# Kernel tuning notes

Measured on AMD Instinct MI355X. Metric: run time of the kernel, lower is better.

## Reference

```python
import jax, jax.numpy as jnp
import numpy as np

B, T, NH, HD = 2, 2048, 12, 128
HIDDEN = NH * HD
EPS = 1.1920928955078125e-07  # torch fp32 finfo eps (F.rms_norm default)


def _rope_cos_sin(T, d_half, base=10000.0):
    inv = 1.0 / (base ** (jnp.arange(d_half, dtype=jnp.float32) / d_half))
    t = jnp.arange(T, dtype=jnp.float32)
    f = t[:, None] * inv[None, :]  # [T, d_half]
    return jnp.cos(f)[None, :, None, :], jnp.sin(f)[None, :, None, :]


def apply_rotary_emb(x, cos, sin):
    d = x.shape[3] // 2
    x1, x2 = x[..., :d], x[..., d:]
    return jnp.concatenate([x1 * cos + x2 * sin, x1 * -sin + x2 * cos], axis=3)


def rms_norm(x):
    return x * jax.lax.rsqrt(jnp.mean(x * x, axis=-1, keepdims=True) + EPS)


def setup_inputs() -> dict:
    key = jax.random.key(0)
    ks = jax.random.split(key, 5)
    x = jax.random.normal(ks[0], (B, T, HIDDEN), dtype=jnp.float32)
    cos, sin = _rope_cos_sin(T, HD // 2)
    s = 1.0 / np.sqrt(HIDDEN)
    Wq = jax.random.normal(ks[1], (HIDDEN, HIDDEN), dtype=jnp.float32) * s
    Wk = jax.random.normal(ks[2], (HIDDEN, HIDDEN), dtype=jnp.float32) * s
    Wv = jax.random.normal(ks[3], (HIDDEN, HIDDEN), dtype=jnp.float32) * s
    Wp = jax.random.normal(ks[4], (HIDDEN, HIDDEN), dtype=jnp.float32) * s
    return {"x": x, "cos": cos, "sin": sin, "Wq": Wq, "Wk": Wk, "Wv": Wv,
            "Wp": Wp, "window": 1024}


def reference(x, cos, sin, Wq, Wk, Wv, Wp, window):
    Bx, Tx, _ = x.shape
    q = (x @ Wq.T).reshape(Bx, Tx, NH, HD)
    k = (x @ Wk.T).reshape(Bx, Tx, NH, HD)
    v = (x @ Wv.T).reshape(Bx, Tx, NH, HD)
    q = rms_norm(apply_rotary_emb(q, cos, sin))
    k = rms_norm(apply_rotary_emb(k, cos, sin))
    # causal + sliding-window attention (dense, matching the sdpa fallback)
    scale = 1.0 / np.sqrt(HD)
    scores = jnp.einsum('bqhd,bkhd->bhqk', q, k) * scale
    row = jnp.arange(Tx)[:, None]
    col = jnp.arange(Tx)[None, :]
    mask = (col <= row) & (row - col <= window)
    scores = jnp.where(mask[None, None], scores, jnp.finfo(scores.dtype).min)
    attn = jax.nn.softmax(scores, axis=-1)
    y = jnp.einsum('bhqk,bkhd->bqhd', attn, v).reshape(Bx, Tx, HIDDEN)
    return y @ Wp.T
```

## Files before the change

### kernel.cpp

```cpp
#include <hip/hip_runtime.h>
#include <stdint.h>

#define HIDDEN 1536
#define NHEAD 12
#define HD 128
#define TSEQ 2048
#define NROWS 4096
#define KDIM HIDDEN
#define EPS_F 1.1920928955078125e-07f
#define SCALE_LOG2E 0.12751879110195655f
#define FIXSUB 16.6f

typedef unsigned short u16;
typedef __bf16 bf16x8_t __attribute__((ext_vector_type(8)));
typedef float f32x4_t __attribute__((ext_vector_type(4)));

#define MFMA16(a, b, c) __builtin_amdgcn_mfma_f32_16x16x32_bf16((a), (b), (c), 0, 0, 0)
#define GLL(srcp, dstp) \
  __builtin_amdgcn_global_load_lds((const __attribute__((address_space(1))) void*)(srcp), \
                                   (__attribute__((address_space(3))) void*)(dstp), 16, 0, 0)

__device__ __forceinline__ u16 f2bf(float f) {
  unsigned u = __builtin_bit_cast(unsigned, f);
  u = (u + 0x7fffu + ((u >> 16) & 1u)) >> 16;
  return (u16)u;
}
__device__ __forceinline__ float bfu(u16 v) {
  return __builtin_bit_cast(float, ((unsigned)v) << 16);
}

__global__ __launch_bounds__(256) void cast_kernel(const float* __restrict__ in,
                                                   u16* __restrict__ out, int n) {
  int i = (blockIdx.x * 256 + threadIdx.x) * 4;
  if (i >= n) return;
  float4 v = *reinterpret_cast<const float4*>(in + i);
  uint2 pk;
  pk.x = (unsigned)f2bf(v.x) | ((unsigned)f2bf(v.y) << 16);
  pk.y = (unsigned)f2bf(v.z) | ((unsigned)f2bf(v.w) << 16);
  *reinterpret_cast<uint2*>(out + i) = pk;
}

__global__ __launch_bounds__(256) void cast4_kernel(
    const float* __restrict__ a, const float* __restrict__ b, const float* __restrict__ c,
    const float* __restrict__ d, u16* __restrict__ oa, u16* __restrict__ ob,
    u16* __restrict__ oc, u16* __restrict__ od, int n) {
  const float* in;
  u16* out;
  switch (blockIdx.y) {
    case 0: in = a; out = oa; break;
    case 1: in = b; out = ob; break;
    case 2: in = c; out = oc; break;
    default: in = d; out = od; break;
  }
  int i = (blockIdx.x * 256 + threadIdx.x) * 4;
  if (i >= n) return;
  float4 v = *reinterpret_cast<const float4*>(in + i);
  uint2 pk;
  pk.x = (unsigned)f2bf(v.x) | ((unsigned)f2bf(v.y) << 16);
  pk.y = (unsigned)f2bf(v.z) | ((unsigned)f2bf(v.w) << 16);
  *reinterpret_cast<uint2*>(out + i) = pk;
}

__device__ __forceinline__ void gemm_mainloop64(const u16* __restrict__ A,
                                                const u16* __restrict__ W, int M0, int N0,
                                                u16* lds, f32x4_t acc[4][4], int tid) {
  const int w = tid >> 6, l = tid & 63;
  const int lrow = l & 15, kg = l >> 4;
  const int wr = (w >> 1) * 64, wc = (w & 1) * 64;
  const int row0 = tid >> 3, j0 = tid & 7;
  const unsigned jsw = (unsigned)((j0 ^ (row0 & 7)) * 8);
  unsigned offA = (unsigned)((M0 + row0) * KDIM) + jsw;
  unsigned offW = (unsigned)((N0 + row0) * KDIM) + jsw;
  const u16* A1 = A + 32 * KDIM; const u16* A2 = A + 64 * KDIM; const u16* A3 = A + 96 * KDIM;
  const u16* W1 = W + 32 * KDIM; const u16* W2 = W + 64 * KDIM; const u16* W3 = W + 96 * KDIM;
  auto issue = [&](int buf) {
    u16* da = lds + buf * 8192 + w * 512;
    u16* dw = lds + 16384 + buf * 8192 + w * 512;
    GLL(A + offA, da);          GLL(A1 + offA, da + 2048);
    GLL(A2 + offA, da + 4096);  GLL(A3 + offA, da + 6144);
    GLL(W + offW, dw);          GLL(W1 + offW, dw + 2048);
    GLL(W2 + offW, dw + 4096);  GLL(W3 + offW, dw + 6144);
    offA += 64; offW += 64;
  };
  issue(0);
  const int NT = KDIM / 64;
#pragma unroll 1
  for (int kt = 0; kt < NT; ++kt) {
    const int cur = kt & 1;
    if (kt + 1 < NT) {
      issue(cur ^ 1);
      asm volatile("s_waitcnt vmcnt(8)" ::: "memory");
    } else {
      asm volatile("s_waitcnt vmcnt(0)" ::: "memory");
    }
    __builtin_amdgcn_s_barrier();
    asm volatile("" ::: "memory");
    const u16* Ab = lds + cur * 8192;
    const u16* Wb = lds + 16384 + cur * 8192;
#pragma unroll
    for (int s = 0; s < 2; ++s) {
      bf16x8_t af[4], bf_[4];
#pragma unroll
      for (int mi = 0; mi < 4; ++mi) {
        const int row = wr + mi * 16 + lrow;
        af[mi] = *reinterpret_cast<const bf16x8_t*>(Ab + row * 64 +
                                                    (((s << 2) | kg) ^ (row & 7)) * 8);
      }
#pragma unroll
      for (int ni = 0; ni < 4; ++ni) {
        const int row = wc + ni * 16 + lrow;
        bf_[ni] = *reinterpret_cast<const bf16x8_t*>(Wb + row * 64 +
                                                     (((s << 2) | kg) ^ (row & 7)) * 8);
      }
#pragma unroll
      for (int mi = 0; mi < 4; ++mi)
#pragma unroll
        for (int ni = 0; ni < 4; ++ni)
          acc[mi][ni] = MFMA16(af[mi], bf_[ni], acc[mi][ni]);
    }
    asm volatile("s_waitcnt lgkmcnt(0)" ::: "memory");
    __builtin_amdgcn_s_barrier();
    asm volatile("" ::: "memory");
  }
}

__global__ __launch_bounds__(256) void gemm_qkv_kernel(
    const u16* __restrict__ xb, const u16* __restrict__ wq, const u16* __restrict__ wk,
    const u16* __restrict__ wv, const float* __restrict__ cosp, const float* __restrict__ sinp,
    u16* __restrict__ qh, u16* __restrict__ kh, u16* __restrict__ vt) {
  __shared__ __align__(16) u16 lds[32768];
  const int tid = threadIdx.x;
  const int wgid = blockIdx.x;
  const int xcd = wgid & 7, c = wgid >> 3;
  const int m = ((xcd & 3) << 3) + (c & 7);
  const int nz = ((xcd >> 2) * 18) + (c >> 3);
  const int z = nz / 12, n = nz % 12;
  const int M0 = m * 128, N0 = n * 128;
  const u16* W = (z == 0) ? wq : (z == 1) ? wk : wv;
  f32x4_t acc[4][4] = {};
  gemm_mainloop64(xb, W, M0, N0, lds, acc, tid);
  const int w = tid >> 6, l = tid & 63;
  const int lrow = l & 15, kg = l >> 4;
  const int wr = (w >> 1) * 64, wc = (w & 1) * 64;
  char* cs = reinterpret_cast<char*>(lds);
  if (z == 2) {
#pragma unroll
    for (int mi = 0; mi < 4; ++mi)
#pragma unroll
      for (int ni = 0; ni < 4; ++ni)
#pragma unroll
        for (int r = 0; r < 4; ++r) {
          const int t_l = wr + mi * 16 + kg * 4 + r;
          const int d = wc + ni * 16 + lrow;
          const int bofs = (d * 256 + t_l * 2) ^ ((d & 7) << 4);
          *reinterpret_cast<u16*>(cs + bofs) = f2bf(acc[mi][ni][r]);
        }
  } else {
#pragma unroll
    for (int mi = 0; mi < 4; ++mi)
#pragma unroll
      for (int ni = 0; ni < 4; ++ni)
#pragma unroll
        for (int r = 0; r < 4; ++r) {
          const int t_l = wr + mi * 16 + kg * 4 + r;
          const int d = wc + ni * 16 + lrow;
          const int bofs = (t_l * 256 + d * 2) ^ ((t_l & 7) << 4);
          *reinterpret_cast<u16*>(cs + bofs) = f2bf(acc[mi][ni][r]);
        }
  }
  __syncthreads();
  const int rr = tid >> 1, hh = tid & 1;
  const int bb = M0 >> 11;
  const int t0 = M0 & (TSEQ - 1);
  const size_t bhn = (size_t)(bb * NHEAD + n);
  if (z == 2) {
    u16* dst = vt + (bhn * HD + rr) * TSEQ + t0 + hh * 64;
    const char* base = cs + rr * 256 + hh * 128;
#pragma unroll
    for (int j = 0; j < 8; ++j) {
      uint4 v = *reinterpret_cast<const uint4*>(base + ((j ^ (rr & 7)) * 16));
      *reinterpret_cast<uint4*>(dst + j * 8) = v;
    }
  } else {
    const int t = t0 + rr;
    const float* cosb = cosp + t * 64;
    const float* sinb = sinp + t * 64;
    const char* base = cs + rr * 256;
    float ss = 0.0f;
    unsigned pk[32];
#pragma unroll
    for (int j = 0; j < 8; ++j) {
      const int jp = (j ^ (rr & 7)) * 16;
      uint4 vo = *reinterpret_cast<const uint4*>(base + hh * 128 + jp);
      uint4 vx = *reinterpret_cast<const uint4*>(base + (hh ^ 1) * 128 + jp);
      const unsigned vo32[4] = {vo.x, vo.y, vo.z, vo.w};
      const unsigned vx32[4] = {vx.x, vx.y, vx.z, vx.w};
      const float* cj = cosb + j * 8;
      const float* sj = sinb + j * 8;
#pragma unroll
      for (int q2 = 0; q2 < 4; ++q2) {
        float o0 = bfu((u16)(vo32[q2] & 0xffffu)), o1 = bfu((u16)(vo32[q2] >> 16));
        float x0 = bfu((u16)(vx32[q2] & 0xffffu)), x1 = bfu((u16)(vx32[q2] >> 16));
        float cc0 = cj[q2 * 2], cc1 = cj[q2 * 2 + 1];
        float s0 = sj[q2 * 2], s1 = sj[q2 * 2 + 1];
        float y0 = hh ? __builtin_fmaf(o0, cc0, -x0 * s0) : __builtin_fmaf(o0, cc0, x0 * s0);
        float y1 = hh ? __builtin_fmaf(o1, cc1, -x1 * s1) : __builtin_fmaf(o1, cc1, x1 * s1);
        ss = __builtin_fmaf(y0, y0, __builtin_fmaf(y1, y1, ss));
        pk[j * 4 + q2] = (unsigned)f2bf(y0) | ((unsigned)f2bf(y1) << 16);
      }
    }
    ss += __shfl_xor(ss, 1, 64);
    const float rinv = rsqrtf(ss * (1.0f / 128.0f) + EPS_F);
    u16* dst = ((z == 0) ? qh : kh) + (bhn * TSEQ + t) * HD + hh * 64;
#pragma unroll
    for (int j = 0; j < 8; ++j) {
      unsigned o[4];
#pragma unroll
      for (int q2 = 0; q2 < 4; ++q2) {
        float y0 = bfu((u16)(pk[j * 4 + q2] & 0xffffu)) * rinv;
        float y1 = bfu((u16)(pk[j * 4 + q2] >> 16)) * rinv;
        o[q2] = (unsigned)f2bf(y0) | ((unsigned)f2bf(y1) << 16);
      }
      uint4 v;
      v.x = o[0]; v.y = o[1]; v.z = o[2]; v.w = o[3];
      *reinterpret_cast<uint4*>(dst + j * 8) = v;
    }
  }
}

__global__ __launch_bounds__(256) void gemm_out_kernel(const u16* __restrict__ yh,
                                                       const u16* __restrict__ wp,
                                                       float* __restrict__ out) {
  __shared__ __align__(16) u16 lds[32768];
  const int tid = threadIdx.x;
  const int wgid = blockIdx.x;
  const int xcd = wgid & 7, c = wgid >> 3;
  const int m = ((xcd & 3) << 3) + (c & 7);
  const int n = ((xcd >> 2) * 6) + (c >> 3);
  const int M0 = m * 128, N0 = n * 128;
  f32x4_t acc[4][4] = {};
  gemm_mainloop64(yh, wp, M0, N0, lds, acc, tid);
  const int w = tid >> 6, l = tid & 63;
  const int lrow = l & 15, kg = l >> 4;
  const int wr = (w >> 1) * 64, wc = (w & 1) * 64;
#pragma unroll
  for (int mi = 0; mi < 4; ++mi)
#pragma unroll
    for (int ni = 0; ni < 4; ++ni)
#pragma unroll
      for (int r = 0; r < 4; ++r) {
        const int grow = M0 + wr + mi * 16 + kg * 4 + r;
        const int gcol = N0 + wc + ni * 16 + lrow;
        out[(size_t)grow * HIDDEN + gcol] = acc[mi][ni][r];
      }
}

__global__ __launch_bounds__(512, 4) void attn_kernel(const u16* __restrict__ qh,
                                                      const u16* __restrict__ kh,
                                                      const u16* __restrict__ vt,
                                                      u16* __restrict__ yh,
                                                      const int* __restrict__ winp) {
  __shared__ __align__(16) u16 Kl[2][8192];
  __shared__ __align__(16) u16 Vl[2][8192];
  __shared__ __align__(16) u16 Pl[8][1024];
  const int tid = threadIdx.x, w = tid >> 6, l = tid & 63;
  const int lrow = l & 15, kg = l >> 4;
  const int bid = blockIdx.x;
  const int swz = (bid & 7) * 48 + (bid >> 3);
  const int qb = swz & 15;
  const int bh = swz >> 4;
  const int h = bh % NHEAD, b = bh / NHEAD;
  const int win = winp[0];
  const u16* Q = qh + (size_t)bh * TSEQ * HD;
  const u16* K = kh + (size_t)bh * TSEQ * HD;
  const u16* V = vt + (size_t)bh * HD * TSEQ;
  const int qw = qb * 128 + w * 16;
  bf16x8_t aq[4];
#pragma unroll
  for (int ks = 0; ks < 4; ++ks)
    aq[ks] = *reinterpret_cast<const bf16x8_t*>(Q + (qw + lrow) * HD + ks * 32 + kg * 8);
  float lsum[4] = {0.f, 0.f, 0.f, 0.f};
  f32x4_t accv[8] = {};
  int lo = qb * 128 - win;
  if (lo < 0) lo = 0;
  lo &= ~63;
  const int last = qb * 128 + 64;

  u16* Pw = &Pl[w][0];

  auto stage_k = [&](int kv, int buf) {
#pragma unroll
    for (int i = 0; i < 2; ++i) {
      const int c = i * 512 + w * 64 + l;
      const int row = c >> 4, j = c & 15;
      const u16* src = K + (size_t)(kv + row) * HD + ((j ^ (row & 7)) * 8);
      GLL(src, &Kl[buf][0] + i * 4096 + w * 512);
    }
  };
  auto stage_v = [&](int kv, int buf) {
#pragma unroll
    for (int i = 0; i < 2; ++i) {
      const int c = i * 512 + w * 64 + l;
      const int row = c >> 3, j = c & 7;
      const u16* src = V + (size_t)row * TSEQ + kv + ((j ^ (row & 7)) * 8);
      GLL(src, &Vl[buf][0] + i * 4096 + w * 512);
    }
  };

  stage_k(lo, 0);
  stage_v(lo, 0);
  int it = 0;
  for (int kv = lo; kv <= last; kv += 64, ++it) {
    const int cur = it & 1;
    const int kpre = (kv + 64 <= last) ? kv + 64 : last;
    stage_k(kpre, cur ^ 1);
    asm volatile("s_waitcnt vmcnt(2)" ::: "memory");
    __builtin_amdgcn_s_barrier();
    asm volatile("" ::: "memory");
    stage_v(kpre, cur ^ 1);
    const u16* Kb = &Kl[cur][0];
    f32x4_t s[4] = {};
#pragma unroll
    for (int n = 0; n < 4; ++n) {
      const int row = n * 16 + lrow;
#pragma unroll
      for (int ks = 0; ks < 4; ++ks) {
        bf16x8_t bk = *reinterpret_cast<const bf16x8_t*>(
            Kb + row * 128 + (((ks << 2) | kg) ^ (row & 7)) * 8);
        s[n] = MFMA16(aq[ks], bk, s[n]);
      }
    }
    float ps[4][4];
    const bool interior = (kv + 63 <= qw) && ((qw + 15) - kv <= win);
    if (interior) {
#pragma unroll
      for (int n = 0; n < 4; ++n)
#pragma unroll
        for (int r = 0; r < 4; ++r)
          ps[n][r] = exp2f(__builtin_fmaf(s[n][r], SCALE_LOG2E, -FIXSUB));
    } else {
#pragma unroll
      for (int n = 0; n < 4; ++n) {
        const int key = kv + n * 16 + lrow;
#pragma unroll
        for (int r = 0; r < 4; ++r) {
          const int rowq = qw + kg * 4 + r;
          const bool ok = (key <= rowq) && (rowq - key <= win);
          ps[n][r] = ok ? exp2f(__builtin_fmaf(s[n][r], SCALE_LOG2E, -FIXSUB)) : 0.0f;
        }
      }
    }
#pragma unroll
    for (int r = 0; r < 4; ++r)
      lsum[r] += (ps[0][r] + ps[1][r]) + (ps[2][r] + ps[3][r]);
#pragma unroll
    for (int n = 0; n < 4; ++n)
#pragma unroll
      for (int r = 0; r < 4; ++r) {
        const int rp = kg * 4 + r;
        int bofs = rp * 128 + (n * 16 + lrow) * 2;
        bofs ^= (rp & 7) << 4;
        *reinterpret_cast<u16*>(reinterpret_cast<char*>(Pw) + bofs) = f2bf(ps[n][r]);
      }
    asm volatile("s_waitcnt lgkmcnt(0)" ::: "memory");
    __builtin_amdgcn_s_barrier();
    asm volatile("" ::: "memory");
    bf16x8_t ap[2];
#pragma unroll
    for (int k2 = 0; k2 < 2; ++k2) {
      int bofs = lrow * 128 + k2 * 64 + kg * 16;
      bofs ^= (lrow & 7) << 4;
      ap[k2] = *reinterpret_cast<const bf16x8_t*>(reinterpret_cast<const char*>(Pw) + bofs);
    }
    const u16* Vb = &Vl[cur][0];
#pragma unroll
    for (int k2 = 0; k2 < 2; ++k2)
#pragma unroll
      for (int dn = 0; dn < 8; ++dn) {
        const int row = dn * 16 + lrow;
        bf16x8_t bv = *reinterpret_cast<const bf16x8_t*>(
            Vb + row * 64 + (((k2 << 2) | kg) ^ (row & 7)) * 8);
        accv[dn] = MFMA16(ap[k2], bv, accv[dn]);
      }
  }
#pragma unroll
  for (int off = 1; off < 16; off <<= 1)
#pragma unroll
    for (int r = 0; r < 4; ++r) lsum[r] += __shfl_xor(lsum[r], off, 64);
  float inv[4];
#pragma unroll
  for (int r = 0; r < 4; ++r) inv[r] = 1.0f / lsum[r];
#pragma unroll
  for (int dn = 0; dn < 8; ++dn)
#pragma unroll
    for (int r = 0; r < 4; ++r) {
      const int rowg = b * TSEQ + qw + kg * 4 + r;
      const int col = h * HD + dn * 16 + lrow;
      yh[(size_t)rowg * HIDDEN + col] = f2bf(accv[dn][r] * inv[r]);
    }
}

extern "C" void kernel_launch(void* const* d_in, const int* in_sizes, int n_in, void* d_out,
                              int out_size, void* d_ws, size_t ws_size, hipStream_t stream) {
  const float* x = (const float*)d_in[0];
  const float* cosp = (const float*)d_in[1];
  const float* sinp = (const float*)d_in[2];
  const float* Wq = (const float*)d_in[3];
  const float* Wk = (const float*)d_in[4];
  const float* Wv = (const float*)d_in[5];
  const float* Wp = (const float*)d_in[6];
  const int* winp = (const int*)d_in[7];

  char* ws = (char*)d_ws;
  size_t off = 0;
  auto alloc = [&](size_t bytes) {
    char* p = ws + off;
    off += (bytes + 255) & ~(size_t)255;
    return p;
  };
  u16* xb = (u16*)alloc((size_t)NROWS * HIDDEN * 2);
  u16* wqb = (u16*)alloc((size_t)HIDDEN * HIDDEN * 2);
  u16* wkb = (u16*)alloc((size_t)HIDDEN * HIDDEN * 2);
  u16* wvb = (u16*)alloc((size_t)HIDDEN * HIDDEN * 2);
  u16* wpb = (u16*)alloc((size_t)HIDDEN * HIDDEN * 2);
  u16* qh = (u16*)alloc((size_t)NROWS * HIDDEN * 2);
  u16* kh = (u16*)alloc((size_t)NROWS * HIDDEN * 2);
  u16* vt = (u16*)alloc((size_t)NROWS * HIDDEN * 2);
  u16* yh = (u16*)alloc((size_t)NROWS * HIDDEN * 2);

  const int nx = NROWS * HIDDEN;
  const int nw = HIDDEN * HIDDEN;
  cast_kernel<<<nx / 1024, 256, 0, stream>>>(x, xb, nx);
  cast4_kernel<<<dim3(nw / 1024, 4), 256, 0, stream>>>(Wq, Wk, Wv, Wp, wqb, wkb, wvb, wpb, nw);

  gemm_qkv_kernel<<<dim3(1152), 256, 0, stream>>>(xb, wqb, wkb, wvb, cosp, sinp, qh, kh, vt);
  attn_kernel<<<dim3(384), 512, 0, stream>>>(qh, kh, vt, yh, winp);
  gemm_out_kernel<<<dim3(384), 256, 0, stream>>>(yh, wpb, (float*)d_out);
}
```

Measured before the change: 185.9 us.

## Rewrite QKV GEMM with 256x128 tiles, 8 waves and split-phase prefetch

The QKV projection GEMM now uses 256x128 output tiles computed by 512-thread blocks (8 waves), halving the grid and reusing each weight tile across twice as many rows. The main loop is split into two MFMA phases, with the global-to-LDS loads for the next tile issued between them and s_setprio raising wave priority during MFMA bursts, so memory traffic overlaps compute. The RoPE/RMSNorm epilogue and the V transpose are adapted to the larger tile. This is meant to cut global/L2 traffic and improve overlap, at the cost of more LDS per block (96 KB) and more barriers per K-step.

```diff
diff --git a/kernel.cpp b/kernel.cpp
--- a/kernel.cpp
+++ b/kernel.cpp
@@ -59,6 +59,192 @@
   pk.x = (unsigned)f2bf(v.x) | ((unsigned)f2bf(v.y) << 16);
   pk.y = (unsigned)f2bf(v.z) | ((unsigned)f2bf(v.w) << 16);
   *reinterpret_cast<uint2*>(out + i) = pk;
+}
+
+__global__ __launch_bounds__(512, 2) void gemm_qkv_kernel(
+    const u16* __restrict__ xb, const u16* __restrict__ wq, const u16* __restrict__ wk,
+    const u16* __restrict__ wv, const float* __restrict__ cosp, const float* __restrict__ sinp,
+    u16* __restrict__ qh, u16* __restrict__ kh, u16* __restrict__ vt) {
+  __shared__ __align__(16) u16 lds[49152];
+  const int tid = threadIdx.x;
+  const int bid = blockIdx.x;
+  const int xcd = bid & 7, cc = bid >> 3;
+  const int m = xcd * 2 + (cc & 1);
+  const int nz = cc >> 1;
+  const int z = nz / 12, n = nz % 12;
+  const int M0 = m * 256, N0 = n * 128;
+  const u16* W = (z == 0) ? wq : (z == 1) ? wk : wv;
+  const int w = tid >> 6, l = tid & 63;
+  const int lrow = l & 15, kg = l >> 4;
+  const int wm = w >> 1, wn = w & 1;
+  const int srow = tid >> 3;
+  const unsigned jsw = (unsigned)(((tid & 7) ^ (srow & 7)) * 8);
+  const u16* pA0 = xb + (size_t)(M0 + srow) * KDIM + jsw;
+  const u16* pA1 = xb + (size_t)(M0 + 128 + srow) * KDIM + jsw;
+  const u16* pB = W + (size_t)(N0 + srow) * KDIM + jsw;
+  const size_t R64 = (size_t)64 * KDIM;
+  u16* dst0 = lds + w * 512;
+  auto stage = [&](const u16* p, int buf, int i) {
+    u16* db = dst0 + buf * 24576 + i * 8192;
+    GLL(p, db);
+    GLL(p + R64, db + 4096);
+  };
+  stage(pA0, 0, 0);
+  stage(pA1, 0, 1);
+  stage(pB, 0, 2);
+  pA0 += 64; pA1 += 64; pB += 64;
+  asm volatile("s_waitcnt vmcnt(0)" ::: "memory");
+  __builtin_amdgcn_s_barrier();
+  asm volatile("" ::: "memory");
+  f32x4_t acc[4][4] = {};
+  const int aoff = (wm >> 1) * 8192;
+  const int arow0 = (wm & 1) * 64;
+  const int swz = lrow & 7;
+  const int NT = KDIM / 64;
+#pragma unroll 1
+  for (int T = 0; T < NT; ++T) {
+    const int buf = T & 1;
+    const u16* Ab = lds + buf * 24576 + aoff;
+    const u16* Bb = lds + buf * 24576 + 16384;
+    bf16x8_t bfr[4][2], afr[2][2];
+#pragma unroll
+    for (int nf = 0; nf < 4; ++nf)
+#pragma unroll
+      for (int ks = 0; ks < 2; ++ks)
+        bfr[nf][ks] = *reinterpret_cast<const bf16x8_t*>(
+            Bb + (wn * 64 + nf * 16 + lrow) * 64 + (((ks << 2) | kg) ^ swz) * 8);
+#pragma unroll
+    for (int mf = 0; mf < 2; ++mf)
+#pragma unroll
+      for (int ks = 0; ks < 2; ++ks)
+        afr[mf][ks] = *reinterpret_cast<const bf16x8_t*>(
+            Ab + (arow0 + mf * 16 + lrow) * 64 + (((ks << 2) | kg) ^ swz) * 8);
+    if (T + 1 < NT) {
+      stage(pA0, buf ^ 1, 0);
+      stage(pA1, buf ^ 1, 1);
+    }
+    __builtin_amdgcn_s_barrier();
+    asm volatile("" ::: "memory");
+    __builtin_amdgcn_s_setprio(1);
+#pragma unroll
+    for (int mf = 0; mf < 2; ++mf)
+#pragma unroll
+      for (int nf = 0; nf < 4; ++nf)
+#pragma unroll
+        for (int ks = 0; ks < 2; ++ks)
+          acc[mf][nf] = MFMA16(afr[mf][ks], bfr[nf][ks], acc[mf][nf]);
+    __builtin_amdgcn_s_setprio(0);
+    __builtin_amdgcn_s_barrier();
+    asm volatile("" ::: "memory");
+    bf16x8_t afr2[2][2];
+#pragma unroll
+    for (int mf = 0; mf < 2; ++mf)
+#pragma unroll
+      for (int ks = 0; ks < 2; ++ks)
+        afr2[mf][ks] = *reinterpret_cast<const bf16x8_t*>(
+            Ab + (arow0 + (mf + 2) * 16 + lrow) * 64 + (((ks << 2) | kg) ^ swz) * 8);
+    if (T + 1 < NT) {
+      stage(pB, buf ^ 1, 2);
+      pA0 += 64; pA1 += 64; pB += 64;
+    }
+    __builtin_amdgcn_s_barrier();
+    asm volatile("" ::: "memory");
+    __builtin_amdgcn_s_setprio(1);
+#pragma unroll
+    for (int mf = 0; mf < 2; ++mf)
+#pragma unroll
+      for (int nf = 0; nf < 4; ++nf)
+#pragma unroll
+        for (int ks = 0; ks < 2; ++ks)
+          acc[mf + 2][nf] = MFMA16(afr2[mf][ks], bfr[nf][ks], acc[mf + 2][nf]);
+    __builtin_amdgcn_s_setprio(0);
+    asm volatile("s_waitcnt vmcnt(0)" ::: "memory");
+    __builtin_amdgcn_s_barrier();
+    asm volatile("" ::: "memory");
+  }
+  char* cs = reinterpret_cast<char*>(lds);
+  const int bb = M0 >> 11;
+  const int t0 = M0 & (TSEQ - 1);
+  const size_t bhn = (size_t)(bb * NHEAD + n);
+  if (z == 2) {
+#pragma unroll
+    for (int mf = 0; mf < 4; ++mf)
+#pragma unroll
+      for (int nf = 0; nf < 4; ++nf)
+#pragma unroll
+        for (int r = 0; r < 4; ++r) {
+          const int trow = wm * 64 + mf * 16 + kg * 4 + r;
+          const int d = wn * 64 + nf * 16 + lrow;
+          const int bofs = (d * 512 + trow * 2) ^ ((d & 7) << 4);
+          *reinterpret_cast<u16*>(cs + bofs) = f2bf(acc[mf][nf][r]);
+        }
+    __syncthreads();
+    const int d = tid >> 2, tq = tid & 3;
+    u16* dst = vt + (bhn * HD + d) * TSEQ + t0 + tq * 64;
+    const char* rb = cs + d * 512 + tq * 128;
+#pragma unroll
+    for (int j = 0; j < 8; ++j) {
+      uint4 v = *reinterpret_cast<const uint4*>(rb + ((j ^ (d & 7)) * 16));
+      *reinterpret_cast<uint4*>(dst + j * 8) = v;
+    }
+  } else {
+#pragma unroll
+    for (int mf = 0; mf < 4; ++mf)
+#pragma unroll
+      for (int nf = 0; nf < 4; ++nf)
+#pragma unroll
+        for (int r = 0; r < 4; ++r) {
+          const int trow = wm * 64 + mf * 16 + kg * 4 + r;
+          const int d = wn * 64 + nf * 16 + lrow;
+          const int bofs = (trow * 256 + d * 2) ^ ((trow & 7) << 4);
+          *reinterpret_cast<u16*>(cs + bofs) = f2bf(acc[mf][nf][r]);
+        }
+    __syncthreads();
+    const int rr = tid >> 1, hh = tid & 1;
+    const int t = t0 + rr;
+    const float* cosb = cosp + t * 64;
+    const float* sinb = sinp + t * 64;
+    const char* base = cs + rr * 256;
+    float ss = 0.0f;
+    unsigned pk[32];
+#pragma unroll
+    for (int j = 0; j < 8; ++j) {
+      const int jp = (j ^ (rr & 7)) * 16;
+      uint4 vo = *reinterpret_cast<const uint4*>(base + hh * 128 + jp);
+      uint4 vx = *reinterpret_cast<const uint4*>(base + (hh ^ 1) * 128 + jp);
+      const unsigned vo32[4] = {vo.x, vo.y, vo.z, vo.w};
+      const unsigned vx32[4] = {vx.x, vx.y, vx.z, vx.w};
+      const float* cj = cosb + j * 8;
+      const float* sj = sinb + j * 8;
+#pragma unroll
+      for (int q2 = 0; q2 < 4; ++q2) {
+        float o0 = bfu((u16)(vo32[q2] & 0xffffu)), o1 = bfu((u16)(vo32[q2] >> 16));
+        float x0 = bfu((u16)(vx32[q2] & 0xffffu)), x1 = bfu((u16)(vx32[q2] >> 16));
+        float cc0 = cj[q2 * 2], cc1 = cj[q2 * 2 + 1];
+        float s0 = sj[q2 * 2], s1 = sj[q2 * 2 + 1];
+        float y0 = hh ? __builtin_fmaf(o0, cc0, -x0 * s0) : __builtin_fmaf(o0, cc0, x0 * s0);
+        float y1 = hh ? __builtin_fmaf(o1, cc1, -x1 * s1) : __builtin_fmaf(o1, cc1, x1 * s1);
+        ss = __builtin_fmaf(y0, y0, __builtin_fmaf(y1, y1, ss));
+        pk[j * 4 + q2] = (unsigned)f2bf(y0) | ((unsigned)f2bf(y1) << 16);
+      }
+    }
+    ss += __shfl_xor(ss, 1, 64);
+    const float rinv = rsqrtf(ss * (1.0f / 128.0f) + EPS_F);
+    u16* dst = ((z == 0) ? qh : kh) + (bhn * TSEQ + t) * HD + hh * 64;
+#pragma unroll
+    for (int j = 0; j < 8; ++j) {
+      unsigned o[4];
+#pragma unroll
+      for (int q2 = 0; q2 < 4; ++q2) {
+        float y0 = bfu((u16)(pk[j * 4 + q2] & 0xffffu)) * rinv;
+        float y1 = bfu((u16)(pk[j * 4 + q2] >> 16)) * rinv;
+        o[q2] = (unsigned)f2bf(y0) | ((unsigned)f2bf(y1) << 16);
+      }
+      uint4 v;
+      v.x = o[0]; v.y = o[1]; v.z = o[2]; v.w = o[3];
+      *reinterpret_cast<uint4*>(dst + j * 8) = v;
+    }
+  }
 }
 
 __device__ __forceinline__ void gemm_mainloop64(const u16* __restrict__ A,
@@ -124,110 +310,6 @@
   }
 }
 
-__global__ __launch_bounds__(256) void gemm_qkv_kernel(
-    const u16* __restrict__ xb, const u16* __restrict__ wq, const u16* __restrict__ wk,
-    const u16* __restrict__ wv, const float* __restrict__ cosp, const float* __restrict__ sinp,
-    u16* __restrict__ qh, u16* __restrict__ kh, u16* __restrict__ vt) {
-  __shared__ __align__(16) u16 lds[32768];
-  const int tid = threadIdx.x;
-  const int wgid = blockIdx.x;
-  const int xcd = wgid & 7, c = wgid >> 3;
-  const int m = ((xcd & 3) << 3) + (c & 7);
-  const int nz = ((xcd >> 2) * 18) + (c >> 3);
-  const int z = nz / 12, n = nz % 12;
-  const int M0 = m * 128, N0 = n * 128;
-  const u16* W = (z == 0) ? wq : (z == 1) ? wk : wv;
-  f32x4_t acc[4][4] = {};
-  gemm_mainloop64(xb, W, M0, N0, lds, acc, tid);
-  const int w = tid >> 6, l = tid & 63;
-  const int lrow = l & 15, kg = l >> 4;
-  const int wr = (w >> 1) * 64, wc = (w & 1) * 64;
-  char* cs = reinterpret_cast<char*>(lds);
-  if (z == 2) {
-#pragma unroll
-    for (int mi = 0; mi < 4; ++mi)
-#pragma unroll
-      for (int ni = 0; ni < 4; ++ni)
-#pragma unroll
-        for (int r = 0; r < 4; ++r) {
-          const int t_l = wr + mi * 16 + kg * 4 + r;
-          const int d = wc + ni * 16 + lrow;
-          const int bofs = (d * 256 + t_l * 2) ^ ((d & 7) << 4);
-          *reinterpret_cast<u16*>(cs + bofs) = f2bf(acc[mi][ni][r]);
-        }
-  } else {
-#pragma unroll
-    for (int mi = 0; mi < 4; ++mi)
-#pragma unroll
-      for (int ni = 0; ni < 4; ++ni)
-#pragma unroll
-        for (int r = 0; r < 4; ++r) {
-          const int t_l = wr + mi * 16 + kg * 4 + r;
-          const int d = wc + ni * 16 + lrow;
-          const int bofs = (t_l * 256 + d * 2) ^ ((t_l & 7) << 4);
-          *reinterpret_cast<u16*>(cs + bofs) = f2bf(acc[mi][ni][r]);
-        }
-  }
-  __syncthreads();
-  const int rr = tid >> 1, hh = tid & 1;
-  const int bb = M0 >> 11;
-  const int t0 = M0 & (TSEQ - 1);
-  const size_t bhn = (size_t)(bb * NHEAD + n);
-  if (z == 2) {
-    u16* dst = vt + (bhn * HD + rr) * TSEQ + t0 + hh * 64;
-    const char* base = cs + rr * 256 + hh * 128;
-#pragma unroll
-    for (int j = 0; j < 8; ++j) {
-      uint4 v = *reinterpret_cast<const uint4*>(base + ((j ^ (rr & 7)) * 16));
-      *reinterpret_cast<uint4*>(dst + j * 8) = v;
-    }
-  } else {
-    const int t = t0 + rr;
-    const float* cosb = cosp + t * 64;
-    const float* sinb = sinp + t * 64;
-    const char* base = cs + rr * 256;
-    float ss = 0.0f;
-    unsigned pk[32];
-#pragma unroll
-    for (int j = 0; j < 8; ++j) {
-      const int jp = (j ^ (rr & 7)) * 16;
-      uint4 vo = *reinterpret_cast<const uint4*>(base + hh * 128 + jp);
-      uint4 vx = *reinterpret_cast<const uint4*>(base + (hh ^ 1) * 128 + jp);
-      const unsigned vo32[4] = {vo.x, vo.y, vo.z, vo.w};
-      const unsigned vx32[4] = {vx.x, vx.y, vx.z, vx.w};
-      const float* cj = cosb + j * 8;
-      const float* sj = sinb + j * 8;
-#pragma unroll
-      for (int q2 = 0; q2 < 4; ++q2) {
-        float o0 = bfu((u16)(vo32[q2] & 0xffffu)), o1 = bfu((u16)(vo32[q2] >> 16));
-        float x0 = bfu((u16)(vx32[q2] & 0xffffu)), x1 = bfu((u16)(vx32[q2] >> 16));
-        float cc0 = cj[q2 * 2], cc1 = cj[q2 * 2 + 1];
-        float s0 = sj[q2 * 2], s1 = sj[q2 * 2 + 1];
-        float y0 = hh ? __builtin_fmaf(o0, cc0, -x0 * s0) : __builtin_fmaf(o0, cc0, x0 * s0);
-        float y1 = hh ? __builtin_fmaf(o1, cc1, -x1 * s1) : __builtin_fmaf(o1, cc1, x1 * s1);
-        ss = __builtin_fmaf(y0, y0, __builtin_fmaf(y1, y1, ss));
-        pk[j * 4 + q2] = (unsigned)f2bf(y0) | ((unsigned)f2bf(y1) << 16);
-      }
-    }
-    ss += __shfl_xor(ss, 1, 64);
-    const float rinv = rsqrtf(ss * (1.0f / 128.0f) + EPS_F);
-    u16* dst = ((z == 0) ? qh : kh) + (bhn * TSEQ + t) * HD + hh * 64;
-#pragma unroll
-    for (int j = 0; j < 8; ++j) {
-      unsigned o[4];
-#pragma unroll
-      for (int q2 = 0; q2 < 4; ++q2) {
-        float y0 = bfu((u16)(pk[j * 4 + q2] & 0xffffu)) * rinv;
-        float y1 = bfu((u16)(pk[j * 4 + q2] >> 16)) * rinv;
-        o[q2] = (unsigned)f2bf(y0) | ((unsigned)f2bf(y1) << 16);
-      }
-      uint4 v;
-      v.x = o[0]; v.y = o[1]; v.z = o[2]; v.w = o[3];
-      *reinterpret_cast<uint4*>(dst + j * 8) = v;
-    }
-  }
-}
-
 __global__ __launch_bounds__(256) void gemm_out_kernel(const u16* __restrict__ yh,
                                                        const u16* __restrict__ wp,
                                                        float* __restrict__ out) {
@@ -433,7 +515,7 @@
   cast_kernel<<<nx / 1024, 256, 0, stream>>>(x, xb, nx);
   cast4_kernel<<<dim3(nw / 1024, 4), 256, 0, stream>>>(Wq, Wk, Wv, Wp, wqb, wkb, wvb, wpb, nw);
 
-  gemm_qkv_kernel<<<dim3(1152), 256, 0, stream>>>(xb, wqb, wkb, wvb, cosp, sinp, qh, kh, vt);
+  gemm_qkv_kernel<<<dim3(576), 512, 0, stream>>>(xb, wqb, wkb, wvb, cosp, sinp, qh, kh, vt);
   attn_kernel<<<dim3(384), 512, 0, stream>>>(qh, kh, vt, yh, winp);
   gemm_out_kernel<<<dim3(384), 256, 0, stream>>>(yh, wpb, (float*)d_out);
 }
```

New measurement: 203.8 us. 1.1x slower.

## Use 8 waves per GEMM block with 64x32 warp tiles

Applied to the files above, without the earlier changes.

Both GEMM kernels move from 4 waves at 64x64 per wave to 8 waves at 64x32 per wave on the same 128x128 tile. Global-to-LDS loads are split over twice as many threads, and the RoPE/RMSNorm and V-transpose epilogues are redistributed across 512 threads with an extra shuffle for the row norm. This halves per-thread accumulators to raise occupancy and latency hiding, at the cost of more LDS fragment reads per MFMA, since A fragments are now reused across only 2 columns.

```diff
diff --git a/kernel.cpp b/kernel.cpp
--- a/kernel.cpp
+++ b/kernel.cpp
@@ -63,24 +63,25 @@
 
 __device__ __forceinline__ void gemm_mainloop64(const u16* __restrict__ A,
                                                 const u16* __restrict__ W, int M0, int N0,
-                                                u16* lds, f32x4_t acc[4][4], int tid) {
+                                                u16* lds, f32x4_t acc[4][2], int tid) {
   const int w = tid >> 6, l = tid & 63;
   const int lrow = l & 15, kg = l >> 4;
-  const int wr = (w >> 1) * 64, wc = (w & 1) * 64;
+  const int wm = w >> 2, wn = w & 3;
+  const int rbase = wm * 64, cbase = wn * 32;
   const int row0 = tid >> 3, j0 = tid & 7;
   const unsigned jsw = (unsigned)((j0 ^ (row0 & 7)) * 8);
   unsigned offA = (unsigned)((M0 + row0) * KDIM) + jsw;
   unsigned offW = (unsigned)((N0 + row0) * KDIM) + jsw;
-  const u16* A1 = A + 32 * KDIM; const u16* A2 = A + 64 * KDIM; const u16* A3 = A + 96 * KDIM;
-  const u16* W1 = W + 32 * KDIM; const u16* W2 = W + 64 * KDIM; const u16* W3 = W + 96 * KDIM;
+  const size_t R64 = (size_t)64 * KDIM;
   auto issue = [&](int buf) {
     u16* da = lds + buf * 8192 + w * 512;
     u16* dw = lds + 16384 + buf * 8192 + w * 512;
-    GLL(A + offA, da);          GLL(A1 + offA, da + 2048);
-    GLL(A2 + offA, da + 4096);  GLL(A3 + offA, da + 6144);
-    GLL(W + offW, dw);          GLL(W1 + offW, dw + 2048);
-    GLL(W2 + offW, dw + 4096);  GLL(W3 + offW, dw + 6144);
-    offA += 64; offW += 64;
+    GLL(A + offA, da);
+    GLL(A + offA + R64, da + 4096);
+    GLL(W + offW, dw);
+    GLL(W + offW + R64, dw + 4096);
+    offA += 64;
+    offW += 64;
   };
   issue(0);
   const int NT = KDIM / 64;
@@ -89,7 +90,7 @@
     const int cur = kt & 1;
     if (kt + 1 < NT) {
       issue(cur ^ 1);
-      asm volatile("s_waitcnt vmcnt(8)" ::: "memory");
+      asm volatile("s_waitcnt vmcnt(4)" ::: "memory");
     } else {
       asm volatile("s_waitcnt vmcnt(0)" ::: "memory");
     }
@@ -99,23 +100,23 @@
     const u16* Wb = lds + 16384 + cur * 8192;
 #pragma unroll
     for (int s = 0; s < 2; ++s) {
-      bf16x8_t af[4], bf_[4];
+      bf16x8_t af[4], bf_[2];
 #pragma unroll
       for (int mi = 0; mi < 4; ++mi) {
-        const int row = wr + mi * 16 + lrow;
+        const int row = rbase + mi * 16 + lrow;
         af[mi] = *reinterpret_cast<const bf16x8_t*>(Ab + row * 64 +
                                                     (((s << 2) | kg) ^ (row & 7)) * 8);
       }
 #pragma unroll
-      for (int ni = 0; ni < 4; ++ni) {
-        const int row = wc + ni * 16 + lrow;
+      for (int ni = 0; ni < 2; ++ni) {
+        const int row = cbase + ni * 16 + lrow;
         bf_[ni] = *reinterpret_cast<const bf16x8_t*>(Wb + row * 64 +
                                                      (((s << 2) | kg) ^ (row & 7)) * 8);
       }
 #pragma unroll
       for (int mi = 0; mi < 4; ++mi)
 #pragma unroll
-        for (int ni = 0; ni < 4; ++ni)
+        for (int ni = 0; ni < 2; ++ni)
           acc[mi][ni] = MFMA16(af[mi], bf_[ni], acc[mi][ni]);
     }
     asm volatile("s_waitcnt lgkmcnt(0)" ::: "memory");
@@ -124,7 +125,7 @@
   }
 }
 
-__global__ __launch_bounds__(256) void gemm_qkv_kernel(
+__global__ __launch_bounds__(512, 4) void gemm_qkv_kernel(
     const u16* __restrict__ xb, const u16* __restrict__ wq, const u16* __restrict__ wk,
     const u16* __restrict__ wv, const float* __restrict__ cosp, const float* __restrict__ sinp,
     u16* __restrict__ qh, u16* __restrict__ kh, u16* __restrict__ vt) {
@@ -137,21 +138,21 @@
   const int z = nz / 12, n = nz % 12;
   const int M0 = m * 128, N0 = n * 128;
   const u16* W = (z == 0) ? wq : (z == 1) ? wk : wv;
-  f32x4_t acc[4][4] = {};
+  f32x4_t acc[4][2] = {};
   gemm_mainloop64(xb, W, M0, N0, lds, acc, tid);
   const int w = tid >> 6, l = tid & 63;
   const int lrow = l & 15, kg = l >> 4;
-  const int wr = (w >> 1) * 64, wc = (w & 1) * 64;
+  const int wm = w >> 2, wn = w & 3;
   char* cs = reinterpret_cast<char*>(lds);
   if (z == 2) {
 #pragma unroll
     for (int mi = 0; mi < 4; ++mi)
 #pragma unroll
-      for (int ni = 0; ni < 4; ++ni)
+      for (int ni = 0; ni < 2; ++ni)
 #pragma unroll
         for (int r = 0; r < 4; ++r) {
-          const int t_l = wr + mi * 16 + kg * 4 + r;
-          const int d = wc + ni * 16 + lrow;
+          const int t_l = wm * 64 + mi * 16 + kg * 4 + r;
+          const int d = wn * 32 + ni * 16 + lrow;
           const int bofs = (d * 256 + t_l * 2) ^ ((d & 7) << 4);
           *reinterpret_cast<u16*>(cs + bofs) = f2bf(acc[mi][ni][r]);
         }
@@ -159,40 +160,44 @@
 #pragma unroll
     for (int mi = 0; mi < 4; ++mi)
 #pragma unroll
-      for (int ni = 0; ni < 4; ++ni)
+      for (int ni = 0; ni < 2; ++ni)
 #pragma unroll
         for (int r = 0; r < 4; ++r) {
-          const int t_l = wr + mi * 16 + kg * 4 + r;
-          const int d = wc + ni * 16 + lrow;
+          const int t_l = wm * 64 + mi * 16 + kg * 4 + r;
+          const int d = wn * 32 + ni * 16 + lrow;
           const int bofs = (t_l * 256 + d * 2) ^ ((t_l & 7) << 4);
           *reinterpret_cast<u16*>(cs + bofs) = f2bf(acc[mi][ni][r]);
         }
   }
   __syncthreads();
-  const int rr = tid >> 1, hh = tid & 1;
   const int bb = M0 >> 11;
   const int t0 = M0 & (TSEQ - 1);
   const size_t bhn = (size_t)(bb * NHEAD + n);
   if (z == 2) {
-    u16* dst = vt + (bhn * HD + rr) * TSEQ + t0 + hh * 64;
-    const char* base = cs + rr * 256 + hh * 128;
-#pragma unroll
-    for (int j = 0; j < 8; ++j) {
-      uint4 v = *reinterpret_cast<const uint4*>(base + ((j ^ (rr & 7)) * 16));
+    const int dd = tid >> 2, tq = tid & 3;
+    u16* dst = vt + (bhn * HD + dd) * TSEQ + t0 + tq * 32;
+    const char* rb = cs + dd * 256;
+#pragma unroll
+    for (int j = 0; j < 4; ++j) {
+      const int jj = tq * 4 + j;
+      uint4 v = *reinterpret_cast<const uint4*>(rb + ((jj ^ (dd & 7)) * 16));
       *reinterpret_cast<uint4*>(dst + j * 8) = v;
     }
   } else {
+    const int rr = tid >> 2, qd = tid & 3;
+    const int hh = qd >> 1;
     const int t = t0 + rr;
-    const float* cosb = cosp + t * 64;
-    const float* sinb = sinp + t * 64;
+    const float* cosb = cosp + t * 64 + (qd & 1) * 32;
+    const float* sinb = sinp + t * 64 + (qd & 1) * 32;
     const char* base = cs + rr * 256;
     float ss = 0.0f;
-    unsigned pk[32];
-#pragma unroll
-    for (int j = 0; j < 8; ++j) {
-      const int jp = (j ^ (rr & 7)) * 16;
-      uint4 vo = *reinterpret_cast<const uint4*>(base + hh * 128 + jp);
-      uint4 vx = *reinterpret_cast<const uint4*>(base + (hh ^ 1) * 128 + jp);
+    unsigned pk[16];
+#pragma unroll
+    for (int j = 0; j < 4; ++j) {
+      const int jo = qd * 4 + j;
+      const int jx = (qd ^ 2) * 4 + j;
+      uint4 vo = *reinterpret_cast<const uint4*>(base + ((jo ^ (rr & 7)) * 16));
+      uint4 vx = *reinterpret_cast<const uint4*>(base + ((jx ^ (rr & 7)) * 16));
       const unsigned vo32[4] = {vo.x, vo.y, vo.z, vo.w};
       const unsigned vx32[4] = {vx.x, vx.y, vx.z, vx.w};
       const float* cj = cosb + j * 8;
@@ -210,10 +215,11 @@
       }
     }
     ss += __shfl_xor(ss, 1, 64);
+    ss += __shfl_xor(ss, 2, 64);
     const float rinv = rsqrtf(ss * (1.0f / 128.0f) + EPS_F);
-    u16* dst = ((z == 0) ? qh : kh) + (bhn * TSEQ + t) * HD + hh * 64;
-#pragma unroll
-    for (int j = 0; j < 8; ++j) {
+    u16* dst = ((z == 0) ? qh : kh) + (bhn * TSEQ + t) * HD + qd * 32;
+#pragma unroll
+    for (int j = 0; j < 4; ++j) {
       unsigned o[4];
 #pragma unroll
       for (int q2 = 0; q2 < 4; ++q2) {
@@ -228,9 +234,9 @@
   }
 }
 
-__global__ __launch_bounds__(256) void gemm_out_kernel(const u16* __restrict__ yh,
-                                                       const u16* __restrict__ wp,
-                                                       float* __restrict__ out) {
+__global__ __launch_bounds__(512, 4) void gemm_out_kernel(const u16* __restrict__ yh,
+                                                          const u16* __restrict__ wp,
+                                                          float* __restrict__ out) {
   __shared__ __align__(16) u16 lds[32768];
   const int tid = threadIdx.x;
   const int wgid = blockIdx.x;
@@ -238,19 +244,19 @@
   const int m = ((xcd & 3) << 3) + (c & 7);
   const int n = ((xcd >> 2) * 6) + (c >> 3);
   const int M0 = m * 128, N0 = n * 128;
-  f32x4_t acc[4][4] = {};
+  f32x4_t acc[4][2] = {};
   gemm_mainloop64(yh, wp, M0, N0, lds, acc, tid);
   const int w = tid >> 6, l = tid & 63;
   const int lrow = l & 15, kg = l >> 4;
-  const int wr = (w >> 1) * 64, wc = (w & 1) * 64;
+  const int wm = w >> 2, wn = w & 3;
 #pragma unroll
   for (int mi = 0; mi < 4; ++mi)
 #pragma unroll
-    for (int ni = 0; ni < 4; ++ni)
+    for (int ni = 0; ni < 2; ++ni)
 #pragma unroll
       for (int r = 0; r < 4; ++r) {
-        const int grow = M0 + wr + mi * 16 + kg * 4 + r;
-        const int gcol = N0 + wc + ni * 16 + lrow;
+        const int grow = M0 + wm * 64 + mi * 16 + kg * 4 + r;
+        const int gcol = N0 + wn * 32 + ni * 16 + lrow;
         out[(size_t)grow * HIDDEN + gcol] = acc[mi][ni][r];
       }
 }
@@ -433,7 +439,7 @@
   cast_kernel<<<nx / 1024, 256, 0, stream>>>(x, xb, nx);
   cast4_kernel<<<dim3(nw / 1024, 4), 256, 0, stream>>>(Wq, Wk, Wv, Wp, wqb, wkb, wvb, wpb, nw);
 
-  gemm_qkv_kernel<<<dim3(1152), 256, 0, stream>>>(xb, wqb, wkb, wvb, cosp, sinp, qh, kh, vt);
+  gemm_qkv_kernel<<<dim3(1152), 512, 0, stream>>>(xb, wqb, wkb, wvb, cosp, sinp, qh, kh, vt);
   attn_kernel<<<dim3(384), 512, 0, stream>>>(qh, kh, vt, yh, winp);
-  gemm_out_kernel<<<dim3(384), 256, 0, stream>>>(yh, wpb, (float*)d_out);
-}
+  gemm_out_kernel<<<dim3(384), 512, 0, stream>>>(yh, wpb, (float*)d_out);
+}
```

New measurement: 185.2 us (median of 2 runs). About the same (-0.4%).
